# Kernel optimization log

Hardware: AMD Instinct MI355X
Metric: run time of the kernel (lower is better)

## Reference

```python
import jax, jax.numpy as jnp
import numpy as np

SCALING = 32.0 / 16.0  # alpha / rank


def setup_inputs() -> dict:
    key = jax.random.key(0)
    k_x, k_w, k_a, k_b, k_m = jax.random.split(key, 5)
    B, S, D_IN, D_OUT, R = 4, 8192, 1024, 1024, 16
    x = jax.random.normal(k_x, (B, S, D_IN), dtype=jnp.float32)
    weight = jax.random.normal(k_w, (D_OUT, D_IN), dtype=jnp.float32) * (1.0 / np.sqrt(D_IN))
    a_w = jax.random.normal(k_a, (R, D_IN), dtype=jnp.float32) * (1.0 / np.sqrt(D_IN))
    b_w = jax.random.normal(k_b, (D_OUT, R), dtype=jnp.float32) * (1.0 / np.sqrt(R))
    magnitude = jax.random.uniform(k_m, (1, D_OUT), dtype=jnp.float32) + 0.5
    return {"x": x, "weight": weight, "a_w": a_w, "b_w": b_w, "magnitude": magnitude}


def reference(x, weight, a_w, b_w, magnitude):
    # Base linear: x @ W^T  -> [B, S, out_dim]
    base_out = jnp.einsum('bsd,od->bso', x, weight)
    # LoRA adapter: scaling * B(A(x)) (dropout p=0 -> identity)
    lora_out = SCALING * jnp.einsum('bsr,or->bso', jnp.einsum('bsd,rd->bsr', x, a_w), b_w)
    # DoRA: reconstruct effective weight, row-norm over in_dim (dim=1)
    w_eff = weight + SCALING * (b_w @ a_w)            # [out_dim, in_dim]
    weight_norm = jnp.linalg.norm(w_eff, axis=1)      # [out_dim] (detached in torch)
    mag_norm_scale = (magnitude / weight_norm).reshape(1, 1, -1)  # broadcast over [B,S,out]
    dora_out = (mag_norm_scale - 1.0) * base_out + mag_norm_scale * lora_out
    # LoRALinear.forward returns base_out + lora branch output
    return base_out + dora_out
```

## Files before the change

### kernel.cpp

```cpp
#include <hip/hip_runtime.h>
#include <hip/hip_bf16.h>


typedef __bf16 bf16x8 __attribute__((ext_vector_type(8)));
typedef __bf16 bf16x4 __attribute__((ext_vector_type(4)));
typedef float  f32x4  __attribute__((ext_vector_type(4)));

#define D_IN  1024
#define D_OUT 1024
#define M_TOT 32768
#define BM 128
#define BN 128
#define BK 32

__device__ __forceinline__ void gl_lds16(const __bf16* g, __bf16* l) {
    __builtin_amdgcn_global_load_lds(
        (const __attribute__((address_space(1))) void*)g,
        (__attribute__((address_space(3))) void*)l,
        16, 0, 0);
}

__global__ void x_to_bf16(const float* __restrict__ x, __bf16* __restrict__ xb) {
    const size_t idx = ((size_t)blockIdx.x * blockDim.x + threadIdx.x) * 8;
    const float4 v0 = *(const float4*)(x + idx);
    const float4 v1 = *(const float4*)(x + idx + 4);
    bf16x8 p = { (__bf16)v0.x, (__bf16)v0.y, (__bf16)v0.z, (__bf16)v0.w,
                 (__bf16)v1.x, (__bf16)v1.y, (__bf16)v1.z, (__bf16)v1.w };
    *(bf16x8*)(xb + idx) = p;
}

__global__ void dora_prep(const float* __restrict__ w,
                          const float* __restrict__ a_w,
                          const float* __restrict__ b_w,
                          const float* __restrict__ mag,
                          __bf16* __restrict__ wb,
                          float* __restrict__ scale) {
    const int o = blockIdx.x;
    const int t = threadIdx.x;

    float bw[16];
#pragma unroll
    for (int r = 0; r < 16; ++r) bw[r] = b_w[o * 16 + r];

    float ss = 0.f;
#pragma unroll
    for (int i = 0; i < 4; ++i) {
        const int k = t + i * 256;
        float dot = 0.f;
#pragma unroll
        for (int r = 0; r < 16; ++r) dot = fmaf(bw[r], a_w[r * D_IN + k], dot);
        const float acc = fmaf(2.0f, dot, w[o * D_IN + k]);
        wb[o * D_IN + k] = (__bf16)acc;
        ss = fmaf(acc, acc, ss);
    }
#pragma unroll
    for (int off = 32; off; off >>= 1) ss += __shfl_down(ss, off, 64);
    __shared__ float wsum[4];
    if ((t & 63) == 0) wsum[t >> 6] = ss;
    __syncthreads();
    if (t == 0) {
        const float tot = wsum[0] + wsum[1] + wsum[2] + wsum[3];
        scale[o] = mag[o] / sqrtf(tot);
    }
}

__global__ void dora_gemm(const __bf16* __restrict__ xb,
                          const __bf16* __restrict__ wb,
                          const float* __restrict__ scale,
                          float* __restrict__ out) {
    __shared__ __bf16 As[BM * BK];
    __shared__ __bf16 Bs[BN * BK];

    const int bx = blockIdx.x;
    const int xcd = bx & 7;
    const int l   = bx >> 3;
    const int bm  = (xcd * 32 + (l >> 3)) * BM;
    const int bn  = (l & 7) * BN;

    const int t  = threadIdx.x;
    const int lane = t & 63;
    const int wave = t >> 6;
    const int wm = (wave & 1) * 64;
    const int wn = (wave >> 1) * 64;
    const int lm = lane & 15;
    const int lq = lane >> 4;

    f32x4 acc[4][4] = {};

    const int srow0 = wave * 32 + (lane >> 2);
    const int scol  = (lane & 3) * 8;
    const __bf16* ag0 = xb + (size_t)(bm + srow0) * D_IN + scol;
    const __bf16* ag1 = ag0 + 16 * D_IN;
    const __bf16* bg0 = wb + (size_t)(bn + srow0) * D_IN + scol;
    const __bf16* bg1 = bg0 + 16 * D_IN;
    __bf16* al0 = As + wave * 1024;
    __bf16* al1 = As + wave * 1024 + 512;
    __bf16* bl0 = Bs + wave * 1024;
    __bf16* bl1 = Bs + wave * 1024 + 512;

    for (int kk = 0; kk < D_IN; kk += BK) {
        gl_lds16(ag0 + kk, al0);
        gl_lds16(ag1 + kk, al1);
        gl_lds16(bg0 + kk, bl0);
        gl_lds16(bg1 + kk, bl1);
        __syncthreads();

        bf16x8 af[4], bfr[4];
#pragma unroll
        for (int i = 0; i < 4; ++i)
            af[i] = *(const bf16x8*)(&As[(wm + i * 16 + lm) * BK + lq * 8]);
#pragma unroll
        for (int i = 0; i < 4; ++i)
            bfr[i] = *(const bf16x8*)(&Bs[(wn + i * 16 + lm) * BK + lq * 8]);

#pragma unroll
        for (int i = 0; i < 4; ++i)
#pragma unroll
            for (int j = 0; j < 4; ++j)
                acc[i][j] = __builtin_amdgcn_mfma_f32_16x16x32_bf16(af[i], bfr[j], acc[i][j], 0, 0, 0);
        __syncthreads();
    }

#pragma unroll
    for (int j = 0; j < 4; ++j) {
        const int n = bn + wn + j * 16 + lm;
        const float sc = scale[n];
#pragma unroll
        for (int i = 0; i < 4; ++i) {
            const int m = bm + wm + i * 16 + lq * 4;
#pragma unroll
            for (int r = 0; r < 4; ++r) {
                out[(size_t)(m + r) * D_OUT + n] = acc[i][j][r] * sc;
            }
        }
    }
}

extern "C" void kernel_launch(void* const* d_in, const int* in_sizes, int n_in,
                              void* d_out, int out_size, void* d_ws, size_t ws_size,
                              hipStream_t stream) {
    const float* x    = (const float*)d_in[0];
    const float* w    = (const float*)d_in[1];
    const float* a_w  = (const float*)d_in[2];
    const float* b_w  = (const float*)d_in[3];
    const float* mag  = (const float*)d_in[4];
    float* out = (float*)d_out;

    __bf16* xb   = (__bf16*)d_ws;
    __bf16* wb   = (__bf16*)((char*)d_ws + (size_t)M_TOT * D_IN * 2);
    float* scale = (float*)((char*)wb + (size_t)D_OUT * D_IN * 2);

    x_to_bf16<<<(M_TOT * D_IN) / (256 * 8), 256, 0, stream>>>(x, xb);
    dora_prep<<<D_OUT, 256, 0, stream>>>(w, a_w, b_w, mag, wb, scale);

    const int grid = (M_TOT / BM) * (D_OUT / BN);
    dora_gemm<<<grid, 256, 0, stream>>>(xb, wb, scale, out);
}
```

Baseline: 314.6 us.

## Fuse fp32-to-bf16 conversion of x into GEMM with double-buffered LDS tiles

Drops the separate x_to_bf16 kernel. The GEMM now loads fp32 x directly, converts it in registers and stores bf16 into LDS. LDS tiles become double-buffered so the next k-tile's global loads overlap the current tile's MFMAs. This removes a full write and re-read of a 64MB bf16 copy of x, but each of the 8 column-blocks now re-reads fp32 x from global/L2 (twice the bytes of the bf16 copy) and adds conversion work inside the GEMM loop.

```diff
diff --git a/kernel.cpp b/kernel.cpp
--- a/kernel.cpp
+++ b/kernel.cpp
@@ -3,7 +3,6 @@
 
 
 typedef __bf16 bf16x8 __attribute__((ext_vector_type(8)));
-typedef __bf16 bf16x4 __attribute__((ext_vector_type(4)));
 typedef float  f32x4  __attribute__((ext_vector_type(4)));
 
 #define D_IN  1024
@@ -12,6 +11,7 @@
 #define BM 128
 #define BN 128
 #define BK 32
+#define NKT (D_IN / BK)
 
 __device__ __forceinline__ void gl_lds16(const __bf16* g, __bf16* l) {
     __builtin_amdgcn_global_load_lds(
@@ -20,13 +20,14 @@
         16, 0, 0);
 }
 
-__global__ void x_to_bf16(const float* __restrict__ x, __bf16* __restrict__ xb) {
-    const size_t idx = ((size_t)blockIdx.x * blockDim.x + threadIdx.x) * 8;
-    const float4 v0 = *(const float4*)(x + idx);
-    const float4 v1 = *(const float4*)(x + idx + 4);
-    bf16x8 p = { (__bf16)v0.x, (__bf16)v0.y, (__bf16)v0.z, (__bf16)v0.w,
-                 (__bf16)v1.x, (__bf16)v1.y, (__bf16)v1.z, (__bf16)v1.w };
-    *(bf16x8*)(xb + idx) = p;
+__device__ __forceinline__ void cvt_store16(__bf16* dst, float4 v0, float4 v1,
+                                            float4 v2, float4 v3) {
+    bf16x8 p0 = { (__bf16)v0.x, (__bf16)v0.y, (__bf16)v0.z, (__bf16)v0.w,
+                  (__bf16)v1.x, (__bf16)v1.y, (__bf16)v1.z, (__bf16)v1.w };
+    bf16x8 p1 = { (__bf16)v2.x, (__bf16)v2.y, (__bf16)v2.z, (__bf16)v2.w,
+                  (__bf16)v3.x, (__bf16)v3.y, (__bf16)v3.z, (__bf16)v3.w };
+    *(bf16x8*)(dst)     = p0;
+    *(bf16x8*)(dst + 8) = p1;
 }
 
 __global__ void dora_prep(const float* __restrict__ w,
@@ -64,12 +65,12 @@
     }
 }
 
-__global__ void dora_gemm(const __bf16* __restrict__ xb,
-                          const __bf16* __restrict__ wb,
-                          const float* __restrict__ scale,
-                          float* __restrict__ out) {
-    __shared__ __bf16 As[BM * BK];
-    __shared__ __bf16 Bs[BN * BK];
+__global__ __launch_bounds__(256) void dora_gemm(const float* __restrict__ x,
+                                                 const __bf16* __restrict__ wb,
+                                                 const float* __restrict__ scale,
+                                                 float* __restrict__ out) {
+    __shared__ __bf16 As[2][BM * BK];
+    __shared__ __bf16 Bs[2][BN * BK];
 
     const int bx = blockIdx.x;
     const int xcd = bx & 7;
@@ -77,7 +78,7 @@
     const int bm  = (xcd * 32 + (l >> 3)) * BM;
     const int bn  = (l & 7) * BN;
 
-    const int t  = threadIdx.x;
+    const int t    = threadIdx.x;
     const int lane = t & 63;
     const int wave = t >> 6;
     const int wm = (wave & 1) * 64;
@@ -85,40 +86,67 @@
     const int lm = lane & 15;
     const int lq = lane >> 4;
 
-    f32x4 acc[4][4] = {};
+    const int arow = t >> 1;
+    const int acol = (t & 1) * 16;
+    const float* ag = x + (size_t)(bm + arow) * D_IN + acol;
+    const int aoff  = arow * BK + acol;
 
     const int srow0 = wave * 32 + (lane >> 2);
     const int scol  = (lane & 3) * 8;
-    const __bf16* ag0 = xb + (size_t)(bm + srow0) * D_IN + scol;
-    const __bf16* ag1 = ag0 + 16 * D_IN;
     const __bf16* bg0 = wb + (size_t)(bn + srow0) * D_IN + scol;
     const __bf16* bg1 = bg0 + 16 * D_IN;
-    __bf16* al0 = As + wave * 1024;
-    __bf16* al1 = As + wave * 1024 + 512;
-    __bf16* bl0 = Bs + wave * 1024;
-    __bf16* bl1 = Bs + wave * 1024 + 512;
+    const int boff0 = wave * 1024;
+    const int boff1 = wave * 1024 + 512;
 
-    for (int kk = 0; kk < D_IN; kk += BK) {
-        gl_lds16(ag0 + kk, al0);
-        gl_lds16(ag1 + kk, al1);
-        gl_lds16(bg0 + kk, bl0);
-        gl_lds16(bg1 + kk, bl1);
-        __syncthreads();
+    f32x4 acc[4][4] = {};
 
+    float4 v0 = *(const float4*)(ag);
+    float4 v1 = *(const float4*)(ag + 4);
+    float4 v2 = *(const float4*)(ag + 8);
+    float4 v3 = *(const float4*)(ag + 12);
+    gl_lds16(bg0, &Bs[0][boff0]);
+    gl_lds16(bg1, &Bs[0][boff1]);
+    cvt_store16(&As[0][aoff], v0, v1, v2, v3);
+    __syncthreads();
+
+    int cur = 0;
+    for (int kt = 0; kt < NKT; ++kt) {
+        const int nxt = cur ^ 1;
+        const bool has_next = (kt + 1) < NKT;
+
+        if (has_next) {
+            const float* agn = ag + (kt + 1) * BK;
+            v0 = *(const float4*)(agn);
+            v1 = *(const float4*)(agn + 4);
+            v2 = *(const float4*)(agn + 8);
+            v3 = *(const float4*)(agn + 12);
+            const __bf16* bgn0 = bg0 + (kt + 1) * BK;
+            const __bf16* bgn1 = bg1 + (kt + 1) * BK;
+            gl_lds16(bgn0, &Bs[nxt][boff0]);
+            gl_lds16(bgn1, &Bs[nxt][boff1]);
+        }
+
+        const __bf16* Ar = As[cur];
+        const __bf16* Br = Bs[cur];
         bf16x8 af[4], bfr[4];
 #pragma unroll
         for (int i = 0; i < 4; ++i)
-            af[i] = *(const bf16x8*)(&As[(wm + i * 16 + lm) * BK + lq * 8]);
+            af[i] = *(const bf16x8*)(&Ar[(wm + i * 16 + lm) * BK + lq * 8]);
 #pragma unroll
         for (int i = 0; i < 4; ++i)
-            bfr[i] = *(const bf16x8*)(&Bs[(wn + i * 16 + lm) * BK + lq * 8]);
+            bfr[i] = *(const bf16x8*)(&Br[(wn + i * 16 + lm) * BK + lq * 8]);
 
 #pragma unroll
         for (int i = 0; i < 4; ++i)
 #pragma unroll
             for (int j = 0; j < 4; ++j)
                 acc[i][j] = __builtin_amdgcn_mfma_f32_16x16x32_bf16(af[i], bfr[j], acc[i][j], 0, 0, 0);
+
+        if (has_next)
+            cvt_store16(&As[nxt][aoff], v0, v1, v2, v3);
+
         __syncthreads();
+        cur = nxt;
     }
 
 #pragma unroll
@@ -146,13 +174,11 @@
     const float* mag  = (const float*)d_in[4];
     float* out = (float*)d_out;
 
-    __bf16* xb   = (__bf16*)d_ws;
-    __bf16* wb   = (__bf16*)((char*)d_ws + (size_t)M_TOT * D_IN * 2);
-    float* scale = (float*)((char*)wb + (size_t)D_OUT * D_IN * 2);
+    __bf16* wb   = (__bf16*)d_ws;
+    float* scale = (float*)((char*)d_ws + (size_t)D_OUT * D_IN * 2);
 
-    x_to_bf16<<<(M_TOT * D_IN) / (256 * 8), 256, 0, stream>>>(x, xb);
     dora_prep<<<D_OUT, 256, 0, stream>>>(w, a_w, b_w, mag, wb, scale);
 
     const int grid = (M_TOT / BM) * (D_OUT / BN);
-    dora_gemm<<<grid, 256, 0, stream>>>(xb, wb, scale, out);
+    dora_gemm<<<grid, 256, 0, stream>>>(x, wb, scale, out);
 }
```

Result: slower. 388.1 us (+23.4%).

## Fuse fp32-to-bf16 conversion of x into GEMM A-tile loads with swizzled LDS

Applied to the files above, without the earlier changes.

Drops the separate x_to_bf16 pass. The GEMM now loads fp32 x tiles straight into LDS, using an XOR-swizzled column layout to avoid bank conflicts, and converts them to bf16 in registers before the MFMA. This removes a full write and reread of the bf16 copy of x (64 MB of traffic plus a launch). In exchange the GEMM's A loads double in bytes, and x is reread from HBM/L2 once per N-tile (8 times), so L2 reuse decides the net effect.

```diff
diff --git a/kernel.cpp b/kernel.cpp
--- a/kernel.cpp
+++ b/kernel.cpp
@@ -3,7 +3,6 @@
 
 
 typedef __bf16 bf16x8 __attribute__((ext_vector_type(8)));
-typedef __bf16 bf16x4 __attribute__((ext_vector_type(4)));
 typedef float  f32x4  __attribute__((ext_vector_type(4)));
 
 #define D_IN  1024
@@ -20,13 +19,11 @@
         16, 0, 0);
 }
 
-__global__ void x_to_bf16(const float* __restrict__ x, __bf16* __restrict__ xb) {
-    const size_t idx = ((size_t)blockIdx.x * blockDim.x + threadIdx.x) * 8;
-    const float4 v0 = *(const float4*)(x + idx);
-    const float4 v1 = *(const float4*)(x + idx + 4);
-    bf16x8 p = { (__bf16)v0.x, (__bf16)v0.y, (__bf16)v0.z, (__bf16)v0.w,
-                 (__bf16)v1.x, (__bf16)v1.y, (__bf16)v1.z, (__bf16)v1.w };
-    *(bf16x8*)(xb + idx) = p;
+__device__ __forceinline__ void gl_lds16f(const float* g, float* l) {
+    __builtin_amdgcn_global_load_lds(
+        (const __attribute__((address_space(1))) void*)g,
+        (__attribute__((address_space(3))) void*)l,
+        16, 0, 0);
 }
 
 __global__ void dora_prep(const float* __restrict__ w,
@@ -64,11 +61,11 @@
     }
 }
 
-__global__ void dora_gemm(const __bf16* __restrict__ xb,
-                          const __bf16* __restrict__ wb,
-                          const float* __restrict__ scale,
-                          float* __restrict__ out) {
-    __shared__ __bf16 As[BM * BK];
+__global__ __launch_bounds__(256) void dora_gemm(const float* __restrict__ x,
+                                                 const __bf16* __restrict__ wb,
+                                                 const float* __restrict__ scale,
+                                                 float* __restrict__ out) {
+    __shared__ float  Asf[BM * BK];
     __shared__ __bf16 Bs[BN * BK];
 
     const int bx = blockIdx.x;
@@ -77,7 +74,7 @@
     const int bm  = (xcd * 32 + (l >> 3)) * BM;
     const int bn  = (l & 7) * BN;
 
-    const int t  = threadIdx.x;
+    const int t    = threadIdx.x;
     const int lane = t & 63;
     const int wave = t >> 6;
     const int wm = (wave & 1) * 64;
@@ -85,33 +82,49 @@
     const int lm = lane & 15;
     const int lq = lane >> 4;
 
-    f32x4 acc[4][4] = {};
+    const int lr = lane >> 3;
+    const int lc = (lane & 7) ^ lr;
+    const float* ag0 = x + (size_t)(bm + wave * 32 +  0 + lr) * D_IN + lc * 4;
+    const float* ag1 = x + (size_t)(bm + wave * 32 +  8 + lr) * D_IN + lc * 4;
+    const float* ag2 = x + (size_t)(bm + wave * 32 + 16 + lr) * D_IN + lc * 4;
+    const float* ag3 = x + (size_t)(bm + wave * 32 + 24 + lr) * D_IN + lc * 4;
+    float* al0 = Asf + wave * 1024;
+    float* al1 = Asf + wave * 1024 + 256;
+    float* al2 = Asf + wave * 1024 + 512;
+    float* al3 = Asf + wave * 1024 + 768;
 
     const int srow0 = wave * 32 + (lane >> 2);
     const int scol  = (lane & 3) * 8;
-    const __bf16* ag0 = xb + (size_t)(bm + srow0) * D_IN + scol;
-    const __bf16* ag1 = ag0 + 16 * D_IN;
     const __bf16* bg0 = wb + (size_t)(bn + srow0) * D_IN + scol;
     const __bf16* bg1 = bg0 + 16 * D_IN;
-    __bf16* al0 = As + wave * 1024;
-    __bf16* al1 = As + wave * 1024 + 512;
     __bf16* bl0 = Bs + wave * 1024;
     __bf16* bl1 = Bs + wave * 1024 + 512;
 
+    f32x4 acc[4][4] = {};
+
     for (int kk = 0; kk < D_IN; kk += BK) {
-        gl_lds16(ag0 + kk, al0);
-        gl_lds16(ag1 + kk, al1);
+        gl_lds16f(ag0 + kk, al0);
+        gl_lds16f(ag1 + kk, al1);
+        gl_lds16f(ag2 + kk, al2);
+        gl_lds16f(ag3 + kk, al3);
         gl_lds16(bg0 + kk, bl0);
         gl_lds16(bg1 + kk, bl1);
         __syncthreads();
 
         bf16x8 af[4], bfr[4];
 #pragma unroll
-        for (int i = 0; i < 4; ++i)
-            af[i] = *(const bf16x8*)(&As[(wm + i * 16 + lm) * BK + lq * 8]);
+        for (int i = 0; i < 4; ++i) {
+            const int r  = wm + i * 16 + lm;
+            const int sw = r & 7;
+            const f32x4 lo = *(const f32x4*)(Asf + r * BK + (((lq * 2)     ^ sw) * 4));
+            const f32x4 hi = *(const f32x4*)(Asf + r * BK + (((lq * 2 + 1) ^ sw) * 4));
+            bf16x8 a8 = { (__bf16)lo.x, (__bf16)lo.y, (__bf16)lo.z, (__bf16)lo.w,
+                          (__bf16)hi.x, (__bf16)hi.y, (__bf16)hi.z, (__bf16)hi.w };
+            af[i] = a8;
+        }
 #pragma unroll
-        for (int i = 0; i < 4; ++i)
-            bfr[i] = *(const bf16x8*)(&Bs[(wn + i * 16 + lm) * BK + lq * 8]);
+        for (int j = 0; j < 4; ++j)
+            bfr[j] = *(const bf16x8*)(&Bs[(wn + j * 16 + lm) * BK + lq * 8]);
 
 #pragma unroll
         for (int i = 0; i < 4; ++i)
@@ -146,13 +159,11 @@
     const float* mag  = (const float*)d_in[4];
     float* out = (float*)d_out;
 
-    __bf16* xb   = (__bf16*)d_ws;
-    __bf16* wb   = (__bf16*)((char*)d_ws + (size_t)M_TOT * D_IN * 2);
-    float* scale = (float*)((char*)wb + (size_t)D_OUT * D_IN * 2);
+    __bf16* wb   = (__bf16*)d_ws;
+    float* scale = (float*)((char*)d_ws + (size_t)D_OUT * D_IN * 2);
 
-    x_to_bf16<<<(M_TOT * D_IN) / (256 * 8), 256, 0, stream>>>(x, xb);
     dora_prep<<<D_OUT, 256, 0, stream>>>(w, a_w, b_w, mag, wb, scale);
 
     const int grid = (M_TOT / BM) * (D_OUT / BN);
-    dora_gemm<<<grid, 256, 0, stream>>>(xb, wb, scale, out);
+    dora_gemm<<<grid, 256, 0, stream>>>(x, wb, scale, out);
 }
```

Result: slower. 352.5 us (+12.0%).
